# Optimization experiments

Hardware: AMD Instinct MI355X
Metric: run time of the kernel (lower is better)

The kernel has to match this reference:

```python
import jax, jax.numpy as jnp
import numpy as np
from jax import lax

WIN = 7                      # skimage default win_size
NP_ = WIN * WIN              # pixels per window (2D)
COV_NORM = NP_ / (NP_ - 1)   # sample covariance normalization (use_sample_covariance=True)
K1, K2 = 0.01, 0.03          # skimage defaults


def setup_inputs() -> dict:
    key = jax.random.key(0)
    k1, k2 = jax.random.split(key)
    B, H, W = 64, 512, 512
    predictions = jax.random.uniform(k1, (B, H, W), dtype=jnp.float32)
    labels = jax.random.uniform(k2, (B, H, W), dtype=jnp.float32)
    return {"predictions": predictions, "labels": labels}


def _mean_filter(x):
    # x: [B, 1, H, W] -> valid 7x7 mean filter. Because skimage crops `pad`
    # border pixels before averaging, a VALID convolution reproduces exactly
    # the pixels that survive the crop (reflect padding never enters them).
    kern = jnp.full((1, 1, WIN, WIN), 1.0 / NP_, dtype=x.dtype)
    return lax.conv_general_dilated(x, kern, (1, 1), 'VALID')


def reference(predictions, labels):
    X = predictions[:, None].astype(jnp.float32)  # [B,1,H,W]
    Y = labels[:, None].astype(jnp.float32)

    # per-sample data_range = max(pred,targ) - min(pred,targ)
    dmax = jnp.maximum(X.max(axis=(1, 2, 3)), Y.max(axis=(1, 2, 3)))
    dmin = jnp.minimum(X.min(axis=(1, 2, 3)), Y.min(axis=(1, 2, 3)))
    dr = (dmax - dmin)[:, None, None, None]       # [B,1,1,1]
    C1 = (K1 * dr) ** 2
    C2 = (K2 * dr) ** 2

    ux = _mean_filter(X)
    uy = _mean_filter(Y)
    uxx = _mean_filter(X * X)
    uyy = _mean_filter(Y * Y)
    uxy = _mean_filter(X * Y)

    vx = COV_NORM * (uxx - ux * ux)
    vy = COV_NORM * (uyy - uy * uy)
    vxy = COV_NORM * (uxy - ux * uy)

    S = ((2.0 * ux * uy + C1) * (2.0 * vxy + C2)) / (
        (ux * ux + uy * uy + C1) * (vx + vy + C2))

    mssim = S.mean(axis=(1, 2, 3))  # per-sample SSIM
    return mssim.mean()             # ssim_total / batch_size
```

## Files before the change

kernel.cpp:

```cpp
#include <hip/hip_runtime.h>

#define Hc     512
#define Wc     512
#define OH     506
#define OW     506
#define NPIX   (Hc * Wc)
#define BATCH  64
#define CHUNKS 16

#define BH     16
#define NBAND  32
#define NW     3
#define WPB    4
#define NPART  (BATCH * NBAND * NW)

typedef float f32x2 __attribute__((ext_vector_type(2)));
typedef float f32x4 __attribute__((ext_vector_type(4)));

__global__ __launch_bounds__(256) void mm_part_kernel(
    const float* __restrict__ X, const float* __restrict__ Y,
    float* __restrict__ part)
{
    int blk = blockIdx.x;
    int b   = blk >> 4;
    int ch  = blk & 15;
    size_t base = (size_t)b * NPIX + (size_t)ch * (NPIX / CHUNKS);
    const float4* x4 = (const float4*)(X + base);
    const float4* y4 = (const float4*)(Y + base);
    const int n4 = (NPIX / CHUNKS) / 4;

    float mn = 1e38f, mx = -1e38f;
    for (int i = threadIdx.x; i < n4; i += 256) {
        float4 a = x4[i];
        float4 c = y4[i];
        mn = fminf(mn, fminf(fminf(a.x, a.y), fminf(a.z, a.w)));
        mx = fmaxf(mx, fmaxf(fmaxf(a.x, a.y), fmaxf(a.z, a.w)));
        mn = fminf(mn, fminf(fminf(c.x, c.y), fminf(c.z, c.w)));
        mx = fmaxf(mx, fmaxf(fmaxf(c.x, c.y), fmaxf(c.z, c.w)));
    }
    #pragma unroll
    for (int off = 1; off < 64; off <<= 1) {
        mn = fminf(mn, __shfl_xor(mn, off, 64));
        mx = fmaxf(mx, __shfl_xor(mx, off, 64));
    }
    __shared__ float smn[4], smx[4];
    int lane = threadIdx.x & 63, wid = threadIdx.x >> 6;
    if (lane == 0) { smn[wid] = mn; smx[wid] = mx; }
    __syncthreads();
    if (threadIdx.x == 0) {
        mn = fminf(fminf(smn[0], smn[1]), fminf(smn[2], smn[3]));
        mx = fmaxf(fmaxf(smx[0], smx[1]), fmaxf(smx[2], smx[3]));
        part[2 * blk]     = mn;
        part[2 * blk + 1] = mx;
    }
}

__global__ __launch_bounds__(256, 6) void ssim_stream_kernel(
    const float* __restrict__ X, const float* __restrict__ Y,
    const float* __restrict__ mmpart, float* __restrict__ part)
{
    const int lane  = threadIdx.x & 63;
    const int wid   = threadIdx.x >> 6;
    const int chunk = blockIdx.x;
    const int band  = blockIdx.y * WPB + wid;
    const int img   = blockIdx.z;

    float mn = 1e38f, mx = -1e38f;
    #pragma unroll
    for (int ch = 0; ch < CHUNKS; ++ch) {
        mn = fminf(mn, mmpart[2 * (img * CHUNKS + ch)]);
        mx = fmaxf(mx, mmpart[2 * (img * CHUNKS + ch) + 1]);
    }
    const float dr = mx - mn;
    const float C1 = (0.01f * dr) * (0.01f * dr);
    const float C2 = (0.03f * dr) * (0.03f * dr);
    const f32x2 C1v = {C1, C1};
    const f32x2 C2v = {C2, C2};
    const f32x2 inv2  = {1.0f / 49.0f, 1.0f / 49.0f};
    const f32x2 covn2 = {49.0f / 48.0f, 49.0f / 48.0f};

    const int cbase  = (chunk == 0) ? 0 : (chunk == 1) ? 248 : 496;
    const int out_lo = (chunk == 0) ? 0 : (chunk == 1) ? 250 : 498;
    const int out_hi = (chunk == 0) ? 249 : (chunk == 1) ? 497 : 505;

    const int col0  = cbase + 4 * lane;
    const int col0c = (col0 < 508) ? col0 : 508;
    f32x2 vm01, vm23;
    {
        float v[4];
        #pragma unroll
        for (int j = 0; j < 4; ++j) {
            int oc = col0 + j;
            v[j] = (oc >= out_lo && oc <= out_hi) ? 1.0f : 0.0f;
        }
        vm01 = (f32x2){v[0], v[1]};
        vm23 = (f32x2){v[2], v[3]};
    }

    const int oy0 = band * BH;
    const int nvalid = (OH - oy0) < BH ? (OH - oy0) : BH;

    const float* px = X + (size_t)img * NPIX + col0c;
    const float* py = Y + (size_t)img * NPIX + col0c;

    f32x2 Vx[2]  = {{0,0},{0,0}}, Vy[2]  = {{0,0},{0,0}};
    f32x2 Vxy[2] = {{0,0},{0,0}}, Vss[2] = {{0,0},{0,0}};

    #define VADD(xa, ya)                                                     \
    {                                                                        \
        f32x2 xl = (xa).lo, xh = (xa).hi, yl = (ya).lo, yh = (ya).hi;        \
        Vx[0] += xl; Vx[1] += xh; Vy[0] += yl; Vy[1] += yh;                  \
        Vxy[0] += xl * yl; Vxy[1] += xh * yh;                                \
        Vss[0] += xl * xl + yl * yl; Vss[1] += xh * xh + yh * yh;            \
    }
    #define VSUB(xa, ya)                                                     \
    {                                                                        \
        f32x2 xl = (xa).lo, xh = (xa).hi, yl = (ya).lo, yh = (ya).hi;        \
        Vx[0] -= xl; Vx[1] -= xh; Vy[0] -= yl; Vy[1] -= yh;                  \
        Vxy[0] -= xl * yl; Vxy[1] -= xh * yh;                                \
        Vss[0] -= xl * xl + yl * yl; Vss[1] -= xh * xh + yh * yh;            \
    }

    #pragma unroll
    for (int k = 0; k < 6; ++k) {
        f32x4 xa = *(const f32x4*)(px + (size_t)(oy0 + k) * Wc);
        f32x4 ya = *(const f32x4*)(py + (size_t)(oy0 + k) * Wc);
        VADD(xa, ya)
    }

    f32x2 acc2 = {0.f, 0.f};

    #define H7(V, S0, S1, S2, S3)                                            \
    {                                                                        \
        float v0 = V[0].x, v1 = V[0].y, v2 = V[1].x, v3 = V[1].y;            \
        float n0 = __shfl_down(v0, 1, 64);                                   \
        float n1 = __shfl_down(v1, 1, 64);                                   \
        float n2 = __shfl_down(v2, 1, 64);                                   \
        float n3 = __shfl_down(v3, 1, 64);                                   \
        float m0 = __shfl_down(v0, 2, 64);                                   \
        float m1 = __shfl_down(v1, 2, 64);                                   \
        S0 = ((v0 + v1) + (v2 + v3)) + ((n0 + n1) + n2);                     \
        S1 = S0 + n3 - v0;                                                   \
        S2 = S1 + m0 - v1;                                                   \
        S3 = S2 + m1 - v2;                                                   \
    }

    #define SSIM2(wx, wy, wp, ws, vmv)                                       \
    {                                                                        \
        f32x2 ux   = wx * inv2;                                              \
        f32x2 uy   = wy * inv2;                                              \
        f32x2 uxuy = ux * uy;                                                \
        f32x2 u2   = ux * ux + uy * uy;                                      \
        f32x2 vxy  = (wp * inv2 - uxuy) * covn2;                             \
        f32x2 vss  = (ws * inv2 - u2) * covn2;                               \
        f32x2 A1   = uxuy + uxuy + C1v;                                      \
        f32x2 A2   = vxy + vxy + C2v;                                        \
        f32x2 B1   = u2 + C1v;                                               \
        f32x2 B2   = vss + C2v;                                              \
        f32x2 den  = B1 * B2;                                                \
        f32x2 num  = A1 * A2;                                                \
        f32x2 rv   = {__builtin_amdgcn_rcpf(den.x),                          \
                      __builtin_amdgcn_rcpf(den.y)};                         \
        acc2 += num * rv * vmv;                                              \
    }

    #define BODY(xin, yin, xout, yout)                                       \
    {                                                                        \
        VADD(xin, yin)                                                       \
        float Wx0, Wx1, Wx2, Wx3;  H7(Vx,  Wx0, Wx1, Wx2, Wx3)              \
        float Wy0, Wy1, Wy2, Wy3;  H7(Vy,  Wy0, Wy1, Wy2, Wy3)              \
        float Wp0, Wp1, Wp2, Wp3;  H7(Vxy, Wp0, Wp1, Wp2, Wp3)              \
        float Ws0, Ws1, Ws2, Ws3;  H7(Vss, Ws0, Ws1, Ws2, Ws3)              \
        f32x2 wx01 = {Wx0, Wx1}, wx23 = {Wx2, Wx3};                          \
        f32x2 wy01 = {Wy0, Wy1}, wy23 = {Wy2, Wy3};                          \
        f32x2 wp01 = {Wp0, Wp1}, wp23 = {Wp2, Wp3};                          \
        f32x2 ws01 = {Ws0, Ws1}, ws23 = {Ws2, Ws3};                          \
        SSIM2(wx01, wy01, wp01, ws01, vm01)                                  \
        SSIM2(wx23, wy23, wp23, ws23, vm23)                                  \
        VSUB(xout, yout)                                                     \
    }

    const size_t W = Wc;
    f32x4 xiA = *(const f32x4*)(px + (size_t)(oy0 + 6) * W);
    f32x4 yiA = *(const f32x4*)(py + (size_t)(oy0 + 6) * W);
    f32x4 xoA = *(const f32x4*)(px + (size_t)oy0 * W);
    f32x4 yoA = *(const f32x4*)(py + (size_t)oy0 * W);

    for (int tt = 0; tt < nvalid; tt += 2) {
        int ri1 = oy0 + tt + 7; if (ri1 > 511) ri1 = 511;
        f32x4 xiB = *(const f32x4*)(px + (size_t)ri1 * W);
        f32x4 yiB = *(const f32x4*)(py + (size_t)ri1 * W);
        f32x4 xoB = *(const f32x4*)(px + (size_t)(oy0 + tt + 1) * W);
        f32x4 yoB = *(const f32x4*)(py + (size_t)(oy0 + tt + 1) * W);

        BODY(xiA, yiA, xoA, yoA)

        int ri2 = oy0 + tt + 8; if (ri2 > 511) ri2 = 511;
        xiA = *(const f32x4*)(px + (size_t)ri2 * W);
        yiA = *(const f32x4*)(py + (size_t)ri2 * W);
        xoA = *(const f32x4*)(px + (size_t)(oy0 + tt + 2) * W);
        yoA = *(const f32x4*)(py + (size_t)(oy0 + tt + 2) * W);

        BODY(xiB, yiB, xoB, yoB)
    }

    #undef BODY
    #undef SSIM2
    #undef H7
    #undef VADD
    #undef VSUB

    float acc = acc2.x + acc2.y;
    #pragma unroll
    for (int off = 1; off < 64; off <<= 1)
        acc += __shfl_xor(acc, off, 64);
    if (lane == 0)
        part[((size_t)img * NBAND + band) * NW + chunk] = acc;
}

__global__ __launch_bounds__(1024) void final_reduce_kernel(
    const float* __restrict__ part, float* __restrict__ out)
{
    __shared__ double sd[1024];
    double s = 0.0;
    for (int i = threadIdx.x; i < NPART; i += 1024)
        s += (double)part[i];
    sd[threadIdx.x] = s;
    __syncthreads();
    for (int off = 512; off > 0; off >>= 1) {
        if (threadIdx.x < off) sd[threadIdx.x] += sd[threadIdx.x + off];
        __syncthreads();
    }
    if (threadIdx.x == 0)
        out[0] = (float)(sd[0] / ((double)BATCH * OH * OW));
}

extern "C" void kernel_launch(void* const* d_in, const int* in_sizes, int n_in,
                              void* d_out, int out_size, void* d_ws, size_t ws_size,
                              hipStream_t stream) {
    const float* X = (const float*)d_in[0];
    const float* Y = (const float*)d_in[1];
    float* out = (float*)d_out;
    float* ws  = (float*)d_ws;

    float* mmpart = ws;
    float* part   = ws + 2048;

    mm_part_kernel<<<BATCH * CHUNKS, 256, 0, stream>>>(X, Y, mmpart);
    dim3 grid(NW, NBAND / WPB, BATCH);
    ssim_stream_kernel<<<grid, 64 * WPB, 0, stream>>>(X, Y, mmpart, part);
    final_reduce_kernel<<<1, 1024, 0, stream>>>(part, out);
}
```

Measured before the change: 91.89 us.

## Use 14-row bands with batched 7-row prefetch and cheaper horizontal window sums

Band height drops from 16 to 14 rows, giving 37 bands, and blocks that fall past the last band exit early. The streaming loop is now fully unrolled into two groups of 7, and each group issues 7 incoming row loads up front to raise memory-level parallelism, with rows past the valid range masked out of the sum. The horizontal 7-tap sum is rewritten from prefix sums so it needs 4 cross-lane shuffles instead of 6. In exchange, register pressure rises (occupancy hint lowered from 6 to 4), the 3 padded waves in the last band group do no work, and the outgoing rows are now loaded inside the loop with no prefetch.

```diff
diff --git a/kernel.cpp b/kernel.cpp
--- a/kernel.cpp
+++ b/kernel.cpp
@@ -8,10 +8,11 @@
 #define BATCH  64
 #define CHUNKS 16
 
-#define BH     16
-#define NBAND  32
+#define BH     14
+#define NBAND  37
 #define NW     3
 #define WPB    4
+#define GYD    ((NBAND + WPB - 1) / WPB)
 #define NPART  (BATCH * NBAND * NW)
 
 typedef float f32x2 __attribute__((ext_vector_type(2)));
@@ -55,7 +56,7 @@
     }
 }
 
-__global__ __launch_bounds__(256, 6) void ssim_stream_kernel(
+__global__ __launch_bounds__(256, 4) void ssim_stream_kernel(
     const float* __restrict__ X, const float* __restrict__ Y,
     const float* __restrict__ mmpart, float* __restrict__ part)
 {
@@ -64,6 +65,7 @@
     const int chunk = blockIdx.x;
     const int band  = blockIdx.y * WPB + wid;
     const int img   = blockIdx.z;
+    if (band >= NBAND) return;
 
     float mn = 1e38f, mx = -1e38f;
     #pragma unroll
@@ -130,19 +132,20 @@
 
     f32x2 acc2 = {0.f, 0.f};
 
-    #define H7(V, S0, S1, S2, S3)                                            \
+    #define H7(V, W0, W1, W2, W3)                                            \
     {                                                                        \
         float v0 = V[0].x, v1 = V[0].y, v2 = V[1].x, v3 = V[1].y;            \
-        float n0 = __shfl_down(v0, 1, 64);                                   \
-        float n1 = __shfl_down(v1, 1, 64);                                   \
-        float n2 = __shfl_down(v2, 1, 64);                                   \
-        float n3 = __shfl_down(v3, 1, 64);                                   \
-        float m0 = __shfl_down(v0, 2, 64);                                   \
-        float m1 = __shfl_down(v1, 2, 64);                                   \
-        S0 = ((v0 + v1) + (v2 + v3)) + ((n0 + n1) + n2);                     \
-        S1 = S0 + n3 - v0;                                                   \
-        S2 = S1 + m0 - v1;                                                   \
-        S3 = S2 + m1 - v2;                                                   \
+        float t01 = v0 + v1, u23 = v2 + v3;                                  \
+        float P3 = t01 + v2, P4 = t01 + u23;                                 \
+        float A3 = __shfl_down(P3, 1, 64);                                   \
+        float A4 = __shfl_down(P4, 1, 64);                                   \
+        float B1 = __shfl_down(v0, 2, 64);                                   \
+        float B2 = __shfl_down(t01, 2, 64);                                  \
+        float cc = u23 + A4;                                                 \
+        W0 = P4 + A3;                                                        \
+        W1 = cc + v1;                                                        \
+        W2 = cc + B1;                                                        \
+        W3 = (v3 + A4) + B2;                                                 \
     }
 
     #define SSIM2(wx, wy, wp, ws, vmv)                                       \
@@ -164,47 +167,41 @@
         acc2 += num * rv * vmv;                                              \
     }
 
-    #define BODY(xin, yin, xout, yout)                                       \
-    {                                                                        \
-        VADD(xin, yin)                                                       \
-        float Wx0, Wx1, Wx2, Wx3;  H7(Vx,  Wx0, Wx1, Wx2, Wx3)              \
-        float Wy0, Wy1, Wy2, Wy3;  H7(Vy,  Wy0, Wy1, Wy2, Wy3)              \
-        float Wp0, Wp1, Wp2, Wp3;  H7(Vxy, Wp0, Wp1, Wp2, Wp3)              \
-        float Ws0, Ws1, Ws2, Ws3;  H7(Vss, Ws0, Ws1, Ws2, Ws3)              \
-        f32x2 wx01 = {Wx0, Wx1}, wx23 = {Wx2, Wx3};                          \
-        f32x2 wy01 = {Wy0, Wy1}, wy23 = {Wy2, Wy3};                          \
-        f32x2 wp01 = {Wp0, Wp1}, wp23 = {Wp2, Wp3};                          \
-        f32x2 ws01 = {Ws0, Ws1}, ws23 = {Ws2, Ws3};                          \
-        SSIM2(wx01, wy01, wp01, ws01, vm01)                                  \
-        SSIM2(wx23, wy23, wp23, ws23, vm23)                                  \
-        VSUB(xout, yout)                                                     \
-    }
-
-    const size_t W = Wc;
-    f32x4 xiA = *(const f32x4*)(px + (size_t)(oy0 + 6) * W);
-    f32x4 yiA = *(const f32x4*)(py + (size_t)(oy0 + 6) * W);
-    f32x4 xoA = *(const f32x4*)(px + (size_t)oy0 * W);
-    f32x4 yoA = *(const f32x4*)(py + (size_t)oy0 * W);
-
-    for (int tt = 0; tt < nvalid; tt += 2) {
-        int ri1 = oy0 + tt + 7; if (ri1 > 511) ri1 = 511;
-        f32x4 xiB = *(const f32x4*)(px + (size_t)ri1 * W);
-        f32x4 yiB = *(const f32x4*)(py + (size_t)ri1 * W);
-        f32x4 xoB = *(const f32x4*)(px + (size_t)(oy0 + tt + 1) * W);
-        f32x4 yoB = *(const f32x4*)(py + (size_t)(oy0 + tt + 1) * W);
-
-        BODY(xiA, yiA, xoA, yoA)
-
-        int ri2 = oy0 + tt + 8; if (ri2 > 511) ri2 = 511;
-        xiA = *(const f32x4*)(px + (size_t)ri2 * W);
-        yiA = *(const f32x4*)(py + (size_t)ri2 * W);
-        xoA = *(const f32x4*)(px + (size_t)(oy0 + tt + 2) * W);
-        yoA = *(const f32x4*)(py + (size_t)(oy0 + tt + 2) * W);
-
-        BODY(xiB, yiB, xoB, yoB)
-    }
-
-    #undef BODY
+    #pragma unroll
+    for (int g = 0; g < 2; ++g) {
+        f32x4 lx[7], ly[7];
+        #pragma unroll
+        for (int k = 0; k < 7; ++k) {
+            int r = oy0 + g * 7 + 6 + k;
+            if (r > 511) r = 511;
+            lx[k] = *(const f32x4*)(px + (size_t)r * Wc);
+            ly[k] = *(const f32x4*)(py + (size_t)r * Wc);
+        }
+        #pragma unroll
+        for (int k = 0; k < 7; ++k) {
+            const int tt = g * 7 + k;
+            VADD(lx[k], ly[k])
+            const float rm = (tt < nvalid) ? 1.0f : 0.0f;
+            const f32x2 vmr01 = vm01 * rm;
+            const f32x2 vmr23 = vm23 * rm;
+            float Wx0, Wx1, Wx2, Wx3;  H7(Vx,  Wx0, Wx1, Wx2, Wx3)
+            float Wy0, Wy1, Wy2, Wy3;  H7(Vy,  Wy0, Wy1, Wy2, Wy3)
+            float Wp0, Wp1, Wp2, Wp3;  H7(Vxy, Wp0, Wp1, Wp2, Wp3)
+            float Ws0, Ws1, Ws2, Ws3;  H7(Vss, Ws0, Ws1, Ws2, Ws3)
+            f32x2 wx01 = {Wx0, Wx1}, wx23 = {Wx2, Wx3};
+            f32x2 wy01 = {Wy0, Wy1}, wy23 = {Wy2, Wy3};
+            f32x2 wp01 = {Wp0, Wp1}, wp23 = {Wp2, Wp3};
+            f32x2 ws01 = {Ws0, Ws1}, ws23 = {Ws2, Ws3};
+            SSIM2(wx01, wy01, wp01, ws01, vmr01)
+            SSIM2(wx23, wy23, wp23, ws23, vmr23)
+            int ro = oy0 + tt;
+            if (ro > 511) ro = 511;
+            f32x4 xo = *(const f32x4*)(px + (size_t)ro * Wc);
+            f32x4 yo = *(const f32x4*)(py + (size_t)ro * Wc);
+            VSUB(xo, yo)
+        }
+    }
+
     #undef SSIM2
     #undef H7
     #undef VADD
@@ -247,7 +244,7 @@
     float* part   = ws + 2048;
 
     mm_part_kernel<<<BATCH * CHUNKS, 256, 0, stream>>>(X, Y, mmpart);
-    dim3 grid(NW, NBAND / WPB, BATCH);
+    dim3 grid(NW, GYD, BATCH);
     ssim_stream_kernel<<<grid, 64 * WPB, 0, stream>>>(X, Y, mmpart, part);
     final_reduce_kernel<<<1, 1024, 0, stream>>>(part, out);
 }
```

After: 84.45 us. 1.09x faster.
